# Performance work log

Measured on AMD Instinct MI355X. Metric: run time of the kernel, lower is better.

Reference implementation:

```python
import jax, jax.numpy as jnp
import numpy as np

TOP_K = 2
SMOOTHING = 0.9


def setup_inputs() -> dict:
    key = jax.random.key(0)
    k1, k2, k3 = jax.random.split(key, 3)
    T, D, E = 16384, 2048, 64
    x = jax.random.normal(k1, (T, D), dtype=jnp.float32)
    gate_w = jax.random.normal(k2, (D, E), dtype=jnp.float32) * (1.0 / np.sqrt(D))
    expert_loads = jax.random.uniform(k3, (E,), dtype=jnp.float32)
    expert_loads = expert_loads / jnp.sum(expert_loads)  # normalized load estimate
    return {"x": x, "gate_w": gate_w, "expert_loads": expert_loads}


def reference(x, gate_w, expert_loads):
    T, _ = x.shape
    E = gate_w.shape[1]
    # Gate projection: [T, D] @ [D, E] -> [T, E]
    logits = jnp.matmul(x, gate_w)
    # Load-balancing bias injection (ExpertLoadBalancer.get_balancing_biases):
    # bias = -(load - 1/E) * 2, added to logits for expert *selection* only.
    biases = -(expert_loads - 1.0 / E) * 2.0
    _, top_idx = jax.lax.top_k(logits + biases[None, :], TOP_K)  # [T, K] int32
    # Routing weights: softmax over the selected (unbiased) logits.
    top_logits = jnp.take_along_axis(logits, top_idx, axis=1)  # [T, K]
    routing_weights = jax.nn.softmax(top_logits, axis=-1)  # [T, K]
    # Vectorized load update (replaces the Python double loop in update_loads):
    # scatter-add routing weights per expert, normalize by token count, EMA-smooth.
    current_loads = jax.ops.segment_sum(
        routing_weights.reshape(-1), top_idx.reshape(-1), num_segments=E
    ) / T
    new_loads = SMOOTHING * expert_loads + (1.0 - SMOOTHING) * current_loads
    return routing_weights, top_idx, new_loads
```

## Files before the change

### kernel.cpp

```cpp
#include <hip/hip_runtime.h>

#define TT 16384
#define DD 2048
#define EE 64

typedef __attribute__((ext_vector_type(8))) short bf16x8;
typedef __attribute__((ext_vector_type(8))) unsigned short ushort8;
typedef __attribute__((ext_vector_type(4))) float f32x4;

__device__ __forceinline__ unsigned short bf16_rne(float f) {
    unsigned u = __float_as_uint(f);
    return (unsigned short)((u + 0x7FFFu + ((u >> 16) & 1u)) >> 16);
}
__device__ __forceinline__ float bf16_f32(unsigned short h) {
    return __uint_as_float(((unsigned)h) << 16);
}
__device__ __forceinline__ unsigned cvt_pk(float lo, float hi) {
    unsigned r;
    asm("v_cvt_pk_bf16_f32 %0, %1, %2" : "=v"(r) : "v"(lo), "v"(hi));
    return r;
}
__device__ __forceinline__ bf16x8 pack4(unsigned a, unsigned b, unsigned c, unsigned d) {
    union { unsigned u[4]; bf16x8 v; } t;
    t.u[0] = a; t.u[1] = b; t.u[2] = c; t.u[3] = d;
    return t.v;
}
__device__ __forceinline__ void gload16(void* lds, const void* g) {
    __builtin_amdgcn_global_load_lds(
        (const __attribute__((address_space(1))) unsigned int*)g,
        (__attribute__((address_space(3))) unsigned int*)lds, 16, 0, 0);
}
#define SB0() __builtin_amdgcn_sched_barrier(0)

__global__ __launch_bounds__(256)
void wconv(const float* __restrict__ wg, unsigned short* __restrict__ wpack) {
    const int t = (int)blockIdx.x * 256 + threadIdx.x;
    const int K0 = t >> 9, h = (t >> 8) & 1, m = (t >> 6) & 3, lane = t & 63;
    const int e = m * 16 + (lane & 15);
    const int ks = K0 * 32 + (lane >> 4) * 8;
    ushort8 v;
#pragma unroll
    for (int j = 0; j < 8; ++j) {
        const float f = wg[(size_t)(ks + j) * EE + e];
        const unsigned short hi = bf16_rne(f);
        v[j] = h ? bf16_rne(f - bf16_f32(hi)) : hi;
    }
    *(ushort8*)(wpack + ((size_t)(K0 * 8 + h * 4 + m) * 64 + lane) * 8) = v;
}

__global__ __launch_bounds__(256, 2)
void gate_fused(const float* __restrict__ x, const unsigned short* __restrict__ wpack,
                const float* __restrict__ loads, float* __restrict__ out,
                float* __restrict__ binpart) {
    __shared__ __align__(16) float arena[12288];
    __shared__ float bins[64];

    const int tid = threadIdx.x, lane = tid & 63, q = tid >> 6;
    const int tb = (int)blockIdx.x;

    f32x4 a0[4] = {{0,0,0,0},{0,0,0,0},{0,0,0,0},{0,0,0,0}};
    f32x4 a1[4] = {{0,0,0,0},{0,0,0,0},{0,0,0,0},{0,0,0,0}};

    float* ring = arena + (size_t)q * 3072;
    float *sp0 = ring, *sp1 = ring + 1024, *sp2 = ring + 2048;

    auto stage_x = [&](int s, float* sb) {
#pragma unroll
        for (int i = 0; i < 4; ++i) {
            const int rowp = lane >> 3;
            const int c = (lane & 7) ^ rowp;
            gload16(sb + i * 256,
                    x + (size_t)(tb * 32 + i * 8 + rowp) * DD + q * 512 + s * 32 + c * 4);
        }
    };
    auto loadW = [&](int s, bf16x8 (&wh)[4], bf16x8 (&wl)[4]) {
        const unsigned short* base = wpack + (size_t)(q * 16 + s) * 4096 + lane * 8;
#pragma unroll
        for (int m = 0; m < 4; ++m) {
            wh[m] = *(const bf16x8*)(base + (size_t)m * 512);
            wl[m] = *(const bf16x8*)(base + (size_t)(4 + m) * 512);
        }
    };
    auto readx = [&](const float* sb, f32x4& va0, f32x4& vb0, f32x4& va1, f32x4& vb1) {
        const int rl = lane & 15;
        const int kgc = (lane >> 4) << 1;
        const int sw = rl & 7;
        va0 = *(const f32x4*)(sb + rl * 32 + ((kgc) ^ sw) * 4);
        vb0 = *(const f32x4*)(sb + rl * 32 + ((kgc + 1) ^ sw) * 4);
        va1 = *(const f32x4*)(sb + (16 + rl) * 32 + ((kgc) ^ sw) * 4);
        vb1 = *(const f32x4*)(sb + (16 + rl) * 32 + ((kgc + 1) ^ sw) * 4);
    };
    auto domfma = [&](const f32x4& va, const f32x4& vb,
                      bf16x8 (&wh)[4], bf16x8 (&wl)[4], f32x4 (&ac)[4]) {
        const float cf[8] = {va.x, va.y, va.z, va.w, vb.x, vb.y, vb.z, vb.w};
        unsigned ph[4], pl[4];
#pragma unroll
        for (int j = 0; j < 4; ++j) {
            ph[j] = cvt_pk(cf[2 * j], cf[2 * j + 1]);
            const float h0 = __uint_as_float(ph[j] << 16);
            const float h1 = __uint_as_float(ph[j] & 0xFFFF0000u);
            pl[j] = cvt_pk(cf[2 * j] - h0, cf[2 * j + 1] - h1);
        }
        const bf16x8 bhi = pack4(ph[0], ph[1], ph[2], ph[3]);
        const bf16x8 blo = pack4(pl[0], pl[1], pl[2], pl[3]);
#pragma unroll
        for (int m = 0; m < 4; ++m) {
            ac[m] = __builtin_amdgcn_mfma_f32_16x16x32_bf16(wh[m], bhi, ac[m], 0, 0, 0);
            ac[m] = __builtin_amdgcn_mfma_f32_16x16x32_bf16(wh[m], blo, ac[m], 0, 0, 0);
            ac[m] = __builtin_amdgcn_mfma_f32_16x16x32_bf16(wl[m], bhi, ac[m], 0, 0, 0);
        }
    };

    bf16x8 WH0[4], WO0[4], WH1[4], WO1[4], WH2[4], WO2[4];

    stage_x(0, sp0); SB0();
    loadW(0, WH0, WO0); SB0();
    stage_x(1, sp1); SB0();
    loadW(1, WH1, WO1); SB0();
    stage_x(2, sp2); SB0();

#define ITER(s, nsl, nwl, VM, DOW, DOS)                                   \
    do {                                                                  \
        asm volatile("s_waitcnt vmcnt(" #VM ")" ::: "memory"); SB0();     \
        f32x4 va0, vb0, va1, vb1;                                         \
        readx(sp##nsl, va0, vb0, va1, vb1); SB0();                        \
        asm volatile("s_waitcnt lgkmcnt(0)" ::: "memory"); SB0();         \
        if (DOW) loadW((s) + 2, WH##nwl, WO##nwl);                        \
        SB0();                                                            \
        if (DOS) stage_x((s) + 3, sp##nsl);                               \
        SB0();                                                            \
        domfma(va0, vb0, WH##nsl, WO##nsl, a0);                           \
        domfma(va1, vb1, WH##nsl, WO##nsl, a1);                           \
    } while (0)

    ITER(0, 0, 2, 16, 1, 1);  ITER(1, 1, 0, 16, 1, 1);
    ITER(2, 2, 1, 16, 1, 1);  ITER(3, 0, 2, 16, 1, 1);
    ITER(4, 1, 0, 16, 1, 1);  ITER(5, 2, 1, 16, 1, 1);
    ITER(6, 0, 2, 16, 1, 1);  ITER(7, 1, 0, 16, 1, 1);
    ITER(8, 2, 1, 16, 1, 1);  ITER(9, 0, 2, 16, 1, 1);
    ITER(10, 1, 0, 16, 1, 1); ITER(11, 2, 1, 16, 1, 1);
    ITER(12, 0, 2, 16, 1, 1);
    ITER(13, 1, 0, 16, 1, 0);
    ITER(14, 2, 0, 12, 0, 0);
    ITER(15, 0, 0, 0, 0, 0);
#undef ITER

    __syncthreads();
    if (q != 0) {
        float* p = arena + (size_t)(q - 1) * 2304 + lane * 36;
#pragma unroll
        for (int m = 0; m < 4; ++m) {
            *(f32x4*)(p + m * 4) = a0[m];
            *(f32x4*)(p + 16 + m * 4) = a1[m];
        }
    }
    __syncthreads();
    if (q != 0) return;

#pragma unroll 1
    for (int qq = 0; qq < 3; ++qq) {
        const float* p = arena + (size_t)qq * 2304 + lane * 36;
#pragma unroll
        for (int m = 0; m < 4; ++m) {
            const f32x4 t0 = *(const f32x4*)(p + m * 4);
            const f32x4 t1 = *(const f32x4*)(p + 16 + m * 4);
            a0[m].x += t0.x; a0[m].y += t0.y; a0[m].z += t0.z; a0[m].w += t0.w;
            a1[m].x += t1.x; a1[m].y += t1.y; a1[m].z += t1.z; a1[m].w += t1.w;
        }
    }

    bins[lane] = 0.0f;
    const int col = lane & 15;
    const int erow = (lane >> 4) * 4;
    auto topk = [&](f32x4 (&r)[4], int tokbase) {
        float v1 = -3.4e38f, u1 = 0.0f, v2 = -3.4e38f, u2 = 0.0f;
        int i1 = 0x7fffffff, i2 = 0x7fffffff;
#pragma unroll
        for (int m = 0; m < 4; ++m)
#pragma unroll
            for (int rr = 0; rr < 4; ++rr) {
                const int e = m * 16 + erow + rr;
                const float u = r[m][rr];
                const float b = u - (loads[e] - 0.015625f) * 2.0f;
                if ((b > v1) || (b == v1 && e < i1)) {
                    v2 = v1; u2 = u1; i2 = i1;
                    v1 = b;  u1 = u;  i1 = e;
                } else if ((b > v2) || (b == v2 && e < i2)) {
                    v2 = b; u2 = u; i2 = e;
                }
            }
#pragma unroll
        for (int s = 0; s < 2; ++s) {
            const int mask = 16 << s;
            const float ov1 = __shfl_xor(v1, mask), ou1 = __shfl_xor(u1, mask);
            const float ov2 = __shfl_xor(v2, mask), ou2 = __shfl_xor(u2, mask);
            const int oi1 = __shfl_xor(i1, mask), oi2 = __shfl_xor(i2, mask);
            if ((ov1 > v1) || (ov1 == v1 && oi1 < i1)) {
                if ((v1 > ov2) || (v1 == ov2 && i1 < oi2)) { v2 = v1; u2 = u1; i2 = i1; }
                else                                        { v2 = ov2; u2 = ou2; i2 = oi2; }
                v1 = ov1; u1 = ou1; i1 = oi1;
            } else if ((ov1 > v2) || (ov1 == v2 && oi1 < i2)) {
                v2 = ov1; u2 = ou1; i2 = oi1;
            }
        }
        if (lane < 16) {
            const int tok = tokbase + col;
            const float mx = fmaxf(u1, u2);
            const float e1 = __expf(u1 - mx), e2 = __expf(u2 - mx);
            const float w1 = e1 / (e1 + e2), w2 = e2 / (e1 + e2);
            *(float2*)(out + 2 * tok) = make_float2(w1, w2);
            *(float2*)(out + 2 * TT + 2 * tok) = make_float2((float)i1, (float)i2);
            atomicAdd(&bins[i1], w1);
            atomicAdd(&bins[i2], w2);
        }
    };
    topk(a0, tb * 32);
    topk(a1, tb * 32 + 16);

    binpart[(size_t)tb * 64 + lane] = bins[lane];
}

__global__ __launch_bounds__(1024)
void finalize(const float* __restrict__ binpart, const float* __restrict__ loads,
              float* __restrict__ out) {
    __shared__ float p[16][64];
    const int e = threadIdx.x & 63, sub = threadIdx.x >> 6;
    float s = 0.0f;
#pragma unroll
    for (int r = 0; r < 32; ++r)
        s += binpart[(size_t)(sub * 32 + r) * 64 + e];
    p[sub][e] = s;
    __syncthreads();
    if (sub == 0) {
        float tot = 0.0f;
#pragma unroll
        for (int k = 0; k < 16; ++k) tot += p[k][e];
        out[4 * TT + e] = 0.9f * loads[e] + 0.1f * (tot * (1.0f / 16384.0f));
    }
}

extern "C" void kernel_launch(void* const* d_in, const int* in_sizes, int n_in,
                              void* d_out, int out_size, void* d_ws, size_t ws_size,
                              hipStream_t stream) {
    const float* x = (const float*)d_in[0];
    const float* wg = (const float*)d_in[1];
    const float* loads = (const float*)d_in[2];
    float* out = (float*)d_out;

    unsigned short* wpack = (unsigned short*)d_ws;
    float* binpart = (float*)(wpack + (size_t)64 * 8 * 64 * 8);

    hipLaunchKernelGGL(wconv, dim3(128), dim3(256), 0, stream, wg, wpack);
    hipLaunchKernelGGL(gate_fused, dim3(512), dim3(256), 0, stream,
                       x, wpack, loads, out, binpart);
    hipLaunchKernelGGL(finalize, dim3(1), dim3(1024), 0, stream,
                       binpart, loads, out);
}
```

Before: 40.19 us.

## Double tokens per block and switch to a two-stage pipeline

Each block now processes 64 tokens with four accumulator sets, halving the grid to 256 blocks and reusing each loaded weight fragment across twice as many tokens. The x staging ring shrinks from three to two larger stages, and weight prefetch moves after the MFMA block. This reduces redundant weight traffic and partial-bin rows, but lowers occupancy to one block per CU and shortens the prefetch distance, risking worse latency hiding on a memory-bound kernel.

Result: slower. 43.35 us (+7.9%).

```diff
diff --git a/kernel.cpp b/kernel.cpp
--- a/kernel.cpp
+++ b/kernel.cpp
@@ -48,11 +48,11 @@
     *(ushort8*)(wpack + ((size_t)(K0 * 8 + h * 4 + m) * 64 + lane) * 8) = v;
 }
 
-__global__ __launch_bounds__(256, 2)
+__global__ __launch_bounds__(256)
 void gate_fused(const float* __restrict__ x, const unsigned short* __restrict__ wpack,
                 const float* __restrict__ loads, float* __restrict__ out,
                 float* __restrict__ binpart) {
-    __shared__ __align__(16) float arena[12288];
+    __shared__ __align__(16) float arena[16384];
     __shared__ float bins[64];
 
     const int tid = threadIdx.x, lane = tid & 63, q = tid >> 6;
@@ -60,17 +60,19 @@
 
     f32x4 a0[4] = {{0,0,0,0},{0,0,0,0},{0,0,0,0},{0,0,0,0}};
     f32x4 a1[4] = {{0,0,0,0},{0,0,0,0},{0,0,0,0},{0,0,0,0}};
-
-    float* ring = arena + (size_t)q * 3072;
-    float *sp0 = ring, *sp1 = ring + 1024, *sp2 = ring + 2048;
+    f32x4 a2[4] = {{0,0,0,0},{0,0,0,0},{0,0,0,0},{0,0,0,0}};
+    f32x4 a3[4] = {{0,0,0,0},{0,0,0,0},{0,0,0,0},{0,0,0,0}};
+
+    float* ring = arena + (size_t)q * 4096;
+    float *sp0 = ring, *sp1 = ring + 2048;
 
     auto stage_x = [&](int s, float* sb) {
 #pragma unroll
-        for (int i = 0; i < 4; ++i) {
+        for (int i = 0; i < 8; ++i) {
             const int rowp = lane >> 3;
             const int c = (lane & 7) ^ rowp;
             gload16(sb + i * 256,
-                    x + (size_t)(tb * 32 + i * 8 + rowp) * DD + q * 512 + s * 32 + c * 4);
+                    x + (size_t)(tb * 64 + i * 8 + rowp) * DD + q * 512 + s * 32 + c * 4);
         }
     };
     auto loadW = [&](int s, bf16x8 (&wh)[4], bf16x8 (&wl)[4]) {
@@ -81,14 +83,12 @@
             wl[m] = *(const bf16x8*)(base + (size_t)(4 + m) * 512);
         }
     };
-    auto readx = [&](const float* sb, f32x4& va0, f32x4& vb0, f32x4& va1, f32x4& vb1) {
+    auto readx = [&](const float* sb, int t, f32x4& va, f32x4& vb) {
         const int rl = lane & 15;
         const int kgc = (lane >> 4) << 1;
         const int sw = rl & 7;
-        va0 = *(const f32x4*)(sb + rl * 32 + ((kgc) ^ sw) * 4);
-        vb0 = *(const f32x4*)(sb + rl * 32 + ((kgc + 1) ^ sw) * 4);
-        va1 = *(const f32x4*)(sb + (16 + rl) * 32 + ((kgc) ^ sw) * 4);
-        vb1 = *(const f32x4*)(sb + (16 + rl) * 32 + ((kgc + 1) ^ sw) * 4);
+        va = *(const f32x4*)(sb + (t * 16 + rl) * 32 + ((kgc) ^ sw) * 4);
+        vb = *(const f32x4*)(sb + (t * 16 + rl) * 32 + ((kgc + 1) ^ sw) * 4);
     };
     auto domfma = [&](const f32x4& va, const f32x4& vb,
                       bf16x8 (&wh)[4], bf16x8 (&wl)[4], f32x4 (&ac)[4]) {
@@ -111,47 +111,53 @@
         }
     };
 
-    bf16x8 WH0[4], WO0[4], WH1[4], WO1[4], WH2[4], WO2[4];
+    bf16x8 WH0[4], WO0[4], WH1[4], WO1[4];
 
     stage_x(0, sp0); SB0();
     loadW(0, WH0, WO0); SB0();
     stage_x(1, sp1); SB0();
     loadW(1, WH1, WO1); SB0();
-    stage_x(2, sp2); SB0();
-
-#define ITER(s, nsl, nwl, VM, DOW, DOS)                                   \
+
+#define ITER(s, sl, ws, VM, DOW, DOS)                                     \
     do {                                                                  \
         asm volatile("s_waitcnt vmcnt(" #VM ")" ::: "memory"); SB0();     \
-        f32x4 va0, vb0, va1, vb1;                                         \
-        readx(sp##nsl, va0, vb0, va1, vb1); SB0();                        \
+        f32x4 va0, vb0, va1, vb1, va2, vb2, va3, vb3;                     \
+        readx(sp##sl, 0, va0, vb0); readx(sp##sl, 1, va1, vb1);           \
+        readx(sp##sl, 2, va2, vb2); readx(sp##sl, 3, va3, vb3);           \
+        SB0();                                                            \
         asm volatile("s_waitcnt lgkmcnt(0)" ::: "memory"); SB0();         \
-        if (DOW) loadW((s) + 2, WH##nwl, WO##nwl);                        \
-        SB0();                                                            \
-        if (DOS) stage_x((s) + 3, sp##nsl);                               \
-        SB0();                                                            \
-        domfma(va0, vb0, WH##nsl, WO##nsl, a0);                           \
-        domfma(va1, vb1, WH##nsl, WO##nsl, a1);                           \
+        if (DOS) stage_x((s) + 2, sp##sl);                                \
+        SB0();                                                            \
+        domfma(va0, vb0, WH##ws, WO##ws, a0);                             \
+        domfma(va1, vb1, WH##ws, WO##ws, a1);                             \
+        domfma(va2, vb2, WH##ws, WO##ws, a2);                             \
+        domfma(va3, vb3, WH##ws, WO##ws, a3);                             \
+        SB0();                                                            \
+        if (DOW) loadW((s) + 2, WH##ws, WO##ws);                          \
+        SB0();                                                            \
     } while (0)
 
-    ITER(0, 0, 2, 16, 1, 1);  ITER(1, 1, 0, 16, 1, 1);
-    ITER(2, 2, 1, 16, 1, 1);  ITER(3, 0, 2, 16, 1, 1);
-    ITER(4, 1, 0, 16, 1, 1);  ITER(5, 2, 1, 16, 1, 1);
-    ITER(6, 0, 2, 16, 1, 1);  ITER(7, 1, 0, 16, 1, 1);
-    ITER(8, 2, 1, 16, 1, 1);  ITER(9, 0, 2, 16, 1, 1);
-    ITER(10, 1, 0, 16, 1, 1); ITER(11, 2, 1, 16, 1, 1);
-    ITER(12, 0, 2, 16, 1, 1);
-    ITER(13, 1, 0, 16, 1, 0);
-    ITER(14, 2, 0, 12, 0, 0);
-    ITER(15, 0, 0, 0, 0, 0);
+    ITER(0, 0, 0, 16, 1, 1);  ITER(1, 1, 1, 16, 1, 1);
+    ITER(2, 0, 0, 16, 1, 1);  ITER(3, 1, 1, 16, 1, 1);
+    ITER(4, 0, 0, 16, 1, 1);  ITER(5, 1, 1, 16, 1, 1);
+    ITER(6, 0, 0, 16, 1, 1);  ITER(7, 1, 1, 16, 1, 1);
+    ITER(8, 0, 0, 16, 1, 1);  ITER(9, 1, 1, 16, 1, 1);
+    ITER(10, 0, 0, 16, 1, 1); ITER(11, 1, 1, 16, 1, 1);
+    ITER(12, 0, 0, 16, 1, 1);
+    ITER(13, 1, 1, 16, 1, 1);
+    ITER(14, 0, 0, 16, 0, 0);
+    ITER(15, 1, 1, 0, 0, 0);
 #undef ITER
 
     __syncthreads();
     if (q != 0) {
-        float* p = arena + (size_t)(q - 1) * 2304 + lane * 36;
-#pragma unroll
-        for (int m = 0; m < 4; ++m) {
-            *(f32x4*)(p + m * 4) = a0[m];
+        float* p = arena + (size_t)(q - 1) * 4352 + lane * 68;
+#pragma unroll
+        for (int m = 0; m < 4; ++m) {
+            *(f32x4*)(p + 0 + m * 4) = a0[m];
             *(f32x4*)(p + 16 + m * 4) = a1[m];
+            *(f32x4*)(p + 32 + m * 4) = a2[m];
+            *(f32x4*)(p + 48 + m * 4) = a3[m];
         }
     }
     __syncthreads();
@@ -159,13 +165,17 @@
 
 #pragma unroll 1
     for (int qq = 0; qq < 3; ++qq) {
-        const float* p = arena + (size_t)qq * 2304 + lane * 36;
-#pragma unroll
-        for (int m = 0; m < 4; ++m) {
-            const f32x4 t0 = *(const f32x4*)(p + m * 4);
+        const float* p = arena + (size_t)qq * 4352 + lane * 68;
+#pragma unroll
+        for (int m = 0; m < 4; ++m) {
+            const f32x4 t0 = *(const f32x4*)(p + 0 + m * 4);
             const f32x4 t1 = *(const f32x4*)(p + 16 + m * 4);
+            const f32x4 t2 = *(const f32x4*)(p + 32 + m * 4);
+            const f32x4 t3 = *(const f32x4*)(p + 48 + m * 4);
             a0[m].x += t0.x; a0[m].y += t0.y; a0[m].z += t0.z; a0[m].w += t0.w;
             a1[m].x += t1.x; a1[m].y += t1.y; a1[m].z += t1.z; a1[m].w += t1.w;
+            a2[m].x += t2.x; a2[m].y += t2.y; a2[m].z += t2.z; a2[m].w += t2.w;
+            a3[m].x += t3.x; a3[m].y += t3.y; a3[m].z += t3.z; a3[m].w += t3.w;
         }
     }
 
@@ -214,8 +224,10 @@
             atomicAdd(&bins[i2], w2);
         }
     };
-    topk(a0, tb * 32);
-    topk(a1, tb * 32 + 16);
+    topk(a0, tb * 64);
+    topk(a1, tb * 64 + 16);
+    topk(a2, tb * 64 + 32);
+    topk(a3, tb * 64 + 48);
 
     binpart[(size_t)tb * 64 + lane] = bins[lane];
 }
@@ -227,8 +239,8 @@
     const int e = threadIdx.x & 63, sub = threadIdx.x >> 6;
     float s = 0.0f;
 #pragma unroll
-    for (int r = 0; r < 32; ++r)
-        s += binpart[(size_t)(sub * 32 + r) * 64 + e];
+    for (int r = 0; r < 16; ++r)
+        s += binpart[(size_t)(sub * 16 + r) * 64 + e];
     p[sub][e] = s;
     __syncthreads();
     if (sub == 0) {
@@ -251,7 +263,7 @@
     float* binpart = (float*)(wpack + (size_t)64 * 8 * 64 * 8);
 
     hipLaunchKernelGGL(wconv, dim3(128), dim3(256), 0, stream, wg, wpack);
-    hipLaunchKernelGGL(gate_fused, dim3(512), dim3(256), 0, stream,
+    hipLaunchKernelGGL(gate_fused, dim3(256), dim3(256), 0, stream,
                        x, wpack, loads, out, binpart);
     hipLaunchKernelGGL(finalize, dim3(1), dim3(1024), 0, stream,
                        binpart, loads, out);
```

## Switch to double-buffered x/W pipeline to fit four blocks per CU

Applied to the files above, without the earlier changes.

Cuts the x staging ring from three LDS slots to two and the W register buffers from three to two, shrinking LDS to 32KB per block. The launch bound rises from 2 to 4 blocks per SM/CU, trading prefetch depth for occupancy. The iteration body is reordered so the W reload for step s+2 is issued after the MFMAs, which reuses the same register slot. Less latency is hidden per wave, so the kernel relies on more resident waves to cover memory latency. Register pressure may force spills.

Result: slower. 61.38 us (+52.7%).

```diff
diff --git a/kernel.cpp b/kernel.cpp
--- a/kernel.cpp
+++ b/kernel.cpp
@@ -48,11 +48,11 @@
     *(ushort8*)(wpack + ((size_t)(K0 * 8 + h * 4 + m) * 64 + lane) * 8) = v;
 }
 
-__global__ __launch_bounds__(256, 2)
+__global__ __launch_bounds__(256, 4)
 void gate_fused(const float* __restrict__ x, const unsigned short* __restrict__ wpack,
                 const float* __restrict__ loads, float* __restrict__ out,
                 float* __restrict__ binpart) {
-    __shared__ __align__(16) float arena[12288];
+    __shared__ __align__(16) float arena[8192];
     __shared__ float bins[64];
 
     const int tid = threadIdx.x, lane = tid & 63, q = tid >> 6;
@@ -61,8 +61,8 @@
     f32x4 a0[4] = {{0,0,0,0},{0,0,0,0},{0,0,0,0},{0,0,0,0}};
     f32x4 a1[4] = {{0,0,0,0},{0,0,0,0},{0,0,0,0},{0,0,0,0}};
 
-    float* ring = arena + (size_t)q * 3072;
-    float *sp0 = ring, *sp1 = ring + 1024, *sp2 = ring + 2048;
+    float* ring = arena + (size_t)q * 2048;
+    float *sp0 = ring, *sp1 = ring + 1024;
 
     auto stage_x = [&](int s, float* sb) {
 #pragma unroll
@@ -111,38 +111,38 @@
         }
     };
 
-    bf16x8 WH0[4], WO0[4], WH1[4], WO1[4], WH2[4], WO2[4];
+    bf16x8 WH0[4], WO0[4], WH1[4], WO1[4];
 
     stage_x(0, sp0); SB0();
     loadW(0, WH0, WO0); SB0();
     stage_x(1, sp1); SB0();
     loadW(1, WH1, WO1); SB0();
-    stage_x(2, sp2); SB0();
-
-#define ITER(s, nsl, nwl, VM, DOW, DOS)                                   \
+
+#define ITER(s, sl, VM, DOW, DOS)                                         \
     do {                                                                  \
         asm volatile("s_waitcnt vmcnt(" #VM ")" ::: "memory"); SB0();     \
         f32x4 va0, vb0, va1, vb1;                                         \
-        readx(sp##nsl, va0, vb0, va1, vb1); SB0();                        \
+        readx(sp##sl, va0, vb0, va1, vb1); SB0();                         \
         asm volatile("s_waitcnt lgkmcnt(0)" ::: "memory"); SB0();         \
-        if (DOW) loadW((s) + 2, WH##nwl, WO##nwl);                        \
+        if (DOS) stage_x((s) + 2, sp##sl);                                \
         SB0();                                                            \
-        if (DOS) stage_x((s) + 3, sp##nsl);                               \
+        domfma(va0, vb0, WH##sl, WO##sl, a0);                             \
+        domfma(va1, vb1, WH##sl, WO##sl, a1);                             \
         SB0();                                                            \
-        domfma(va0, vb0, WH##nsl, WO##nsl, a0);                           \
-        domfma(va1, vb1, WH##nsl, WO##nsl, a1);                           \
+        if (DOW) loadW((s) + 2, WH##sl, WO##sl);                          \
+        SB0();                                                            \
     } while (0)
 
-    ITER(0, 0, 2, 16, 1, 1);  ITER(1, 1, 0, 16, 1, 1);
-    ITER(2, 2, 1, 16, 1, 1);  ITER(3, 0, 2, 16, 1, 1);
-    ITER(4, 1, 0, 16, 1, 1);  ITER(5, 2, 1, 16, 1, 1);
-    ITER(6, 0, 2, 16, 1, 1);  ITER(7, 1, 0, 16, 1, 1);
-    ITER(8, 2, 1, 16, 1, 1);  ITER(9, 0, 2, 16, 1, 1);
-    ITER(10, 1, 0, 16, 1, 1); ITER(11, 2, 1, 16, 1, 1);
-    ITER(12, 0, 2, 16, 1, 1);
-    ITER(13, 1, 0, 16, 1, 0);
-    ITER(14, 2, 0, 12, 0, 0);
-    ITER(15, 0, 0, 0, 0, 0);
+    ITER(0, 0, 12, 1, 1);  ITER(1, 1, 12, 1, 1);
+    ITER(2, 0, 12, 1, 1);  ITER(3, 1, 12, 1, 1);
+    ITER(4, 0, 12, 1, 1);  ITER(5, 1, 12, 1, 1);
+    ITER(6, 0, 12, 1, 1);  ITER(7, 1, 12, 1, 1);
+    ITER(8, 0, 12, 1, 1);  ITER(9, 1, 12, 1, 1);
+    ITER(10, 0, 12, 1, 1); ITER(11, 1, 12, 1, 1);
+    ITER(12, 0, 12, 1, 1);
+    ITER(13, 1, 12, 1, 1);
+    ITER(14, 0, 12, 0, 0);
+    ITER(15, 1, 0, 0, 0);
 #undef ITER
 
     __syncthreads();
```

## Share gate weights via LDS across two token groups per 512-thread block

Applied to the files above, without the earlier changes.

Doubles the block to 512 threads covering 64 tokens, with two warps per K-quarter sharing bf16 hi/lo weight tiles. The tiles are staged into double-buffered LDS with async loads instead of each warp loading them into registers from global memory. This halves global weight traffic per token and frees registers, but adds two block-wide barriers per K-step and uses far more LDS, which caps occupancy at one block per CU. The finalize kernel is adjusted for 256 partial bins.

Result: no change. 40.85 us (+1.6%).

```diff
diff --git a/kernel.cpp b/kernel.cpp
--- a/kernel.cpp
+++ b/kernel.cpp
@@ -48,20 +48,21 @@
     *(ushort8*)(wpack + ((size_t)(K0 * 8 + h * 4 + m) * 64 + lane) * 8) = v;
 }
 
-__global__ __launch_bounds__(256, 2)
+__global__ __launch_bounds__(512, 1)
 void gate_fused(const float* __restrict__ x, const unsigned short* __restrict__ wpack,
                 const float* __restrict__ loads, float* __restrict__ out,
                 float* __restrict__ binpart) {
-    __shared__ __align__(16) float arena[12288];
-    __shared__ float bins[64];
-
-    const int tid = threadIdx.x, lane = tid & 63, q = tid >> 6;
+    __shared__ __align__(16) float arena[24576];
+    __shared__ __align__(16) float wlds[16384];
+
+    const int tid = threadIdx.x, lane = tid & 63, w = tid >> 6;
+    const int q = w >> 1, tg = w & 1;
     const int tb = (int)blockIdx.x;
 
     f32x4 a0[4] = {{0,0,0,0},{0,0,0,0},{0,0,0,0},{0,0,0,0}};
     f32x4 a1[4] = {{0,0,0,0},{0,0,0,0},{0,0,0,0},{0,0,0,0}};
 
-    float* ring = arena + (size_t)q * 3072;
+    float* ring = arena + (size_t)w * 3072;
     float *sp0 = ring, *sp1 = ring + 1024, *sp2 = ring + 2048;
 
     auto stage_x = [&](int s, float* sb) {
@@ -70,15 +71,25 @@
             const int rowp = lane >> 3;
             const int c = (lane & 7) ^ rowp;
             gload16(sb + i * 256,
-                    x + (size_t)(tb * 32 + i * 8 + rowp) * DD + q * 512 + s * 32 + c * 4);
-        }
-    };
-    auto loadW = [&](int s, bf16x8 (&wh)[4], bf16x8 (&wl)[4]) {
-        const unsigned short* base = wpack + (size_t)(q * 16 + s) * 4096 + lane * 8;
+                    x + (size_t)(tb * 64 + tg * 32 + i * 8 + rowp) * DD
+                      + q * 512 + s * 32 + c * 4);
+        }
+    };
+    auto stage_W = [&](int s, int slot) {
+        const unsigned short* srcb =
+            wpack + (size_t)(q * 16 + s) * 4096 + (size_t)(tg * 4) * 512 + lane * 8;
+        float* db = wlds + (size_t)slot * 8192 + q * 2048 + tg * 4 * 256;
+#pragma unroll
+        for (int j = 0; j < 4; ++j)
+            gload16(db + j * 256, srcb + (size_t)j * 512);
+    };
+    auto readW = [&](int slot, bf16x8 (&wh)[4], bf16x8 (&wl)[4]) {
+        const unsigned short* b = (const unsigned short*)wlds
+            + (size_t)slot * 16384 + q * 4096 + lane * 8;
 #pragma unroll
         for (int m = 0; m < 4; ++m) {
-            wh[m] = *(const bf16x8*)(base + (size_t)m * 512);
-            wl[m] = *(const bf16x8*)(base + (size_t)(4 + m) * 512);
+            wh[m] = *(const bf16x8*)(b + (size_t)m * 512);
+            wl[m] = *(const bf16x8*)(b + (size_t)(4 + m) * 512);
         }
     };
     auto readx = [&](const float* sb, f32x4& va0, f32x4& vb0, f32x4& va1, f32x4& vb1) {
@@ -111,113 +122,117 @@
         }
     };
 
-    bf16x8 WH0[4], WO0[4], WH1[4], WO1[4], WH2[4], WO2[4];
-
+    stage_W(0, 0); SB0();
     stage_x(0, sp0); SB0();
-    loadW(0, WH0, WO0); SB0();
+    stage_W(1, 1); SB0();
     stage_x(1, sp1); SB0();
-    loadW(1, WH1, WO1); SB0();
     stage_x(2, sp2); SB0();
 
-#define ITER(s, nsl, nwl, VM, DOW, DOS)                                   \
+#define ITER(s, XS, WS, VM, DOW, DOS)                                     \
     do {                                                                  \
         asm volatile("s_waitcnt vmcnt(" #VM ")" ::: "memory"); SB0();     \
+        __builtin_amdgcn_s_barrier(); SB0();                              \
         f32x4 va0, vb0, va1, vb1;                                         \
-        readx(sp##nsl, va0, vb0, va1, vb1); SB0();                        \
+        bf16x8 wh[4], wl[4];                                              \
+        readx(sp##XS, va0, vb0, va1, vb1);                                \
+        readW(WS, wh, wl); SB0();                                         \
         asm volatile("s_waitcnt lgkmcnt(0)" ::: "memory"); SB0();         \
-        if (DOW) loadW((s) + 2, WH##nwl, WO##nwl);                        \
+        __builtin_amdgcn_s_barrier(); SB0();                              \
+        if (DOW) stage_W((s) + 2, ((s) + 2) & 1);                         \
         SB0();                                                            \
-        if (DOS) stage_x((s) + 3, sp##nsl);                               \
+        if (DOS) stage_x((s) + 3, sp##XS);                                \
         SB0();                                                            \
-        domfma(va0, vb0, WH##nsl, WO##nsl, a0);                           \
-        domfma(va1, vb1, WH##nsl, WO##nsl, a1);                           \
+        domfma(va0, vb0, wh, wl, a0);                                     \
+        domfma(va1, vb1, wh, wl, a1);                                     \
     } while (0)
 
-    ITER(0, 0, 2, 16, 1, 1);  ITER(1, 1, 0, 16, 1, 1);
-    ITER(2, 2, 1, 16, 1, 1);  ITER(3, 0, 2, 16, 1, 1);
-    ITER(4, 1, 0, 16, 1, 1);  ITER(5, 2, 1, 16, 1, 1);
-    ITER(6, 0, 2, 16, 1, 1);  ITER(7, 1, 0, 16, 1, 1);
-    ITER(8, 2, 1, 16, 1, 1);  ITER(9, 0, 2, 16, 1, 1);
-    ITER(10, 1, 0, 16, 1, 1); ITER(11, 2, 1, 16, 1, 1);
-    ITER(12, 0, 2, 16, 1, 1);
-    ITER(13, 1, 0, 16, 1, 0);
-    ITER(14, 2, 0, 12, 0, 0);
-    ITER(15, 0, 0, 0, 0, 0);
+    ITER(0, 0, 0, 12, 1, 1);  ITER(1, 1, 1, 12, 1, 1);
+    ITER(2, 2, 0, 12, 1, 1);  ITER(3, 0, 1, 12, 1, 1);
+    ITER(4, 1, 0, 12, 1, 1);  ITER(5, 2, 1, 12, 1, 1);
+    ITER(6, 0, 0, 12, 1, 1);  ITER(7, 1, 1, 12, 1, 1);
+    ITER(8, 2, 0, 12, 1, 1);  ITER(9, 0, 1, 12, 1, 1);
+    ITER(10, 1, 0, 12, 1, 1); ITER(11, 2, 1, 12, 1, 1);
+    ITER(12, 0, 0, 12, 1, 1);
+    ITER(13, 1, 1, 12, 1, 0);
+    ITER(14, 2, 0, 8, 0, 0);
+    ITER(15, 0, 1, 0, 0, 0);
 #undef ITER
 
+    float* binsp = arena;
+    float* ovbase = arena + 64;
     __syncthreads();
     if (q != 0) {
-        float* p = arena + (size_t)(q - 1) * 2304 + lane * 36;
+        float* p = ovbase + (size_t)((q - 1) * 2 + tg) * 2304 + lane * 36;
 #pragma unroll
         for (int m = 0; m < 4; ++m) {
             *(f32x4*)(p + m * 4) = a0[m];
             *(f32x4*)(p + 16 + m * 4) = a1[m];
         }
     }
-    __syncthreads();
-    if (q != 0) return;
-
+    if (w == 0) binsp[lane] = 0.0f;
+    __syncthreads();
+
+    if (q == 0) {
 #pragma unroll 1
-    for (int qq = 0; qq < 3; ++qq) {
-        const float* p = arena + (size_t)qq * 2304 + lane * 36;
-#pragma unroll
-        for (int m = 0; m < 4; ++m) {
-            const f32x4 t0 = *(const f32x4*)(p + m * 4);
-            const f32x4 t1 = *(const f32x4*)(p + 16 + m * 4);
-            a0[m].x += t0.x; a0[m].y += t0.y; a0[m].z += t0.z; a0[m].w += t0.w;
-            a1[m].x += t1.x; a1[m].y += t1.y; a1[m].z += t1.z; a1[m].w += t1.w;
-        }
-    }
-
-    bins[lane] = 0.0f;
-    const int col = lane & 15;
-    const int erow = (lane >> 4) * 4;
-    auto topk = [&](f32x4 (&r)[4], int tokbase) {
-        float v1 = -3.4e38f, u1 = 0.0f, v2 = -3.4e38f, u2 = 0.0f;
-        int i1 = 0x7fffffff, i2 = 0x7fffffff;
-#pragma unroll
-        for (int m = 0; m < 4; ++m)
-#pragma unroll
-            for (int rr = 0; rr < 4; ++rr) {
-                const int e = m * 16 + erow + rr;
-                const float u = r[m][rr];
-                const float b = u - (loads[e] - 0.015625f) * 2.0f;
-                if ((b > v1) || (b == v1 && e < i1)) {
-                    v2 = v1; u2 = u1; i2 = i1;
-                    v1 = b;  u1 = u;  i1 = e;
-                } else if ((b > v2) || (b == v2 && e < i2)) {
-                    v2 = b; u2 = u; i2 = e;
+        for (int qq = 0; qq < 3; ++qq) {
+            const float* p = ovbase + (size_t)(qq * 2 + tg) * 2304 + lane * 36;
+#pragma unroll
+            for (int m = 0; m < 4; ++m) {
+                const f32x4 t0 = *(const f32x4*)(p + m * 4);
+                const f32x4 t1 = *(const f32x4*)(p + 16 + m * 4);
+                a0[m].x += t0.x; a0[m].y += t0.y; a0[m].z += t0.z; a0[m].w += t0.w;
+                a1[m].x += t1.x; a1[m].y += t1.y; a1[m].z += t1.z; a1[m].w += t1.w;
+            }
+        }
+        const int col = lane & 15;
+        const int erow = (lane >> 4) * 4;
+        auto topk = [&](f32x4 (&r)[4], int tokbase) {
+            float v1 = -3.4e38f, u1 = 0.0f, v2 = -3.4e38f, u2 = 0.0f;
+            int i1 = 0x7fffffff, i2 = 0x7fffffff;
+#pragma unroll
+            for (int m = 0; m < 4; ++m)
+#pragma unroll
+                for (int rr = 0; rr < 4; ++rr) {
+                    const int e = m * 16 + erow + rr;
+                    const float u = r[m][rr];
+                    const float b = u - (loads[e] - 0.015625f) * 2.0f;
+                    if ((b > v1) || (b == v1 && e < i1)) {
+                        v2 = v1; u2 = u1; i2 = i1;
+                        v1 = b;  u1 = u;  i1 = e;
+                    } else if ((b > v2) || (b == v2 && e < i2)) {
+                        v2 = b; u2 = u; i2 = e;
+                    }
+                }
+#pragma unroll
+            for (int s = 0; s < 2; ++s) {
+                const int mask = 16 << s;
+                const float ov1 = __shfl_xor(v1, mask), ou1 = __shfl_xor(u1, mask);
+                const float ov2 = __shfl_xor(v2, mask), ou2 = __shfl_xor(u2, mask);
+                const int oi1 = __shfl_xor(i1, mask), oi2 = __shfl_xor(i2, mask);
+                if ((ov1 > v1) || (ov1 == v1 && oi1 < i1)) {
+                    if ((v1 > ov2) || (v1 == ov2 && i1 < oi2)) { v2 = v1; u2 = u1; i2 = i1; }
+                    else                                        { v2 = ov2; u2 = ou2; i2 = oi2; }
+                    v1 = ov1; u1 = ou1; i1 = oi1;
+                } else if ((ov1 > v2) || (ov1 == v2 && oi1 < i2)) {
+                    v2 = ov1; u2 = ou1; i2 = oi1;
                 }
             }
-#pragma unroll
-        for (int s = 0; s < 2; ++s) {
-            const int mask = 16 << s;
-            const float ov1 = __shfl_xor(v1, mask), ou1 = __shfl_xor(u1, mask);
-            const float ov2 = __shfl_xor(v2, mask), ou2 = __shfl_xor(u2, mask);
-            const int oi1 = __shfl_xor(i1, mask), oi2 = __shfl_xor(i2, mask);
-            if ((ov1 > v1) || (ov1 == v1 && oi1 < i1)) {
-                if ((v1 > ov2) || (v1 == ov2 && i1 < oi2)) { v2 = v1; u2 = u1; i2 = i1; }
-                else                                        { v2 = ov2; u2 = ou2; i2 = oi2; }
-                v1 = ov1; u1 = ou1; i1 = oi1;
-            } else if ((ov1 > v2) || (ov1 == v2 && oi1 < i2)) {
-                v2 = ov1; u2 = ou1; i2 = oi1;
+            if (lane < 16) {
+                const int tok = tokbase + col;
+                const float mx = fmaxf(u1, u2);
+                const float e1 = __expf(u1 - mx), e2 = __expf(u2 - mx);
+                const float w1 = e1 / (e1 + e2), w2 = e2 / (e1 + e2);
+                *(float2*)(out + 2 * tok) = make_float2(w1, w2);
+                *(float2*)(out + 2 * TT + 2 * tok) = make_float2((float)i1, (float)i2);
+                atomicAdd(&binsp[i1], w1);
+                atomicAdd(&binsp[i2], w2);
             }
-        }
-        if (lane < 16) {
-            const int tok = tokbase + col;
-            const float mx = fmaxf(u1, u2);
-            const float e1 = __expf(u1 - mx), e2 = __expf(u2 - mx);
-            const float w1 = e1 / (e1 + e2), w2 = e2 / (e1 + e2);
-            *(float2*)(out + 2 * tok) = make_float2(w1, w2);
-            *(float2*)(out + 2 * TT + 2 * tok) = make_float2((float)i1, (float)i2);
-            atomicAdd(&bins[i1], w1);
-            atomicAdd(&bins[i2], w2);
-        }
-    };
-    topk(a0, tb * 32);
-    topk(a1, tb * 32 + 16);
-
-    binpart[(size_t)tb * 64 + lane] = bins[lane];
+        };
+        topk(a0, tb * 64 + tg * 32);
+        topk(a1, tb * 64 + tg * 32 + 16);
+    }
+    __syncthreads();
+    if (w == 0) binpart[(size_t)tb * 64 + lane] = binsp[lane];
 }
 
 __global__ __launch_bounds__(1024)
@@ -227,8 +242,8 @@
     const int e = threadIdx.x & 63, sub = threadIdx.x >> 6;
     float s = 0.0f;
 #pragma unroll
-    for (int r = 0; r < 32; ++r)
-        s += binpart[(size_t)(sub * 32 + r) * 64 + e];
+    for (int r = 0; r < 16; ++r)
+        s += binpart[(size_t)(sub * 16 + r) * 64 + e];
     p[sub][e] = s;
     __syncthreads();
     if (sub == 0) {
@@ -251,7 +266,7 @@
     float* binpart = (float*)(wpack + (size_t)64 * 8 * 64 * 8);
 
     hipLaunchKernelGGL(wconv, dim3(128), dim3(256), 0, stream, wg, wpack);
-    hipLaunchKernelGGL(gate_fused, dim3(512), dim3(256), 0, stream,
+    hipLaunchKernelGGL(gate_fused, dim3(256), dim3(512), 0, stream,
                        x, wpack, loads, out, binpart);
     hipLaunchKernelGGL(finalize, dim3(1), dim3(1024), 0, stream,
                        binpart, loads, out);
```
